# Kernel tuning notes

Hardware: AMD Instinct MI355X
Metric: run time of the kernel (lower is better)

The kernel has to match this reference:

```python
import jax, jax.numpy as jnp
import numpy as np

D_MODEL = 2048
N_HEADS = 16
HEAD_DIM = 128
WINDOW = 512
ROPE_BASE = 10000.0
B, N = 2, 2048
INNER = N_HEADS * HEAD_DIM


def setup_inputs() -> dict:
    key = jax.random.key(0)
    k1, k2, k3 = jax.random.split(key, 3)
    x = jax.random.normal(k1, (B, N, D_MODEL), dtype=jnp.float32)
    # torch nn.Linear stores weight as [out_features, in_features]
    w_qkv = jax.random.normal(k2, (3 * INNER, D_MODEL), dtype=jnp.float32) / np.sqrt(D_MODEL)
    w_o = jax.random.normal(k3, (D_MODEL, INNER), dtype=jnp.float32) / np.sqrt(INNER)
    return {"x": x, "w_qkv": w_qkv, "w_o": w_o}


def _rotate_half(t):
    t1, t2 = jnp.split(t, 2, axis=-1)
    return jnp.concatenate([-t2, t1], axis=-1)


def _rope(q, k, offset=0):
    # q, k: [B, H, N, D]; GPT-NeoX half-split rotary embedding
    D = q.shape[-1]
    inv_freq = 1.0 / (ROPE_BASE ** (jnp.arange(0, D, 2, dtype=jnp.float32) / D))
    pos = jnp.arange(q.shape[2], dtype=jnp.float32) + offset
    ang = pos[:, None] * inv_freq[None, :]                 # [N, D/2]
    cos = jnp.concatenate([jnp.cos(ang), jnp.cos(ang)], axis=-1)  # [N, D]
    sin = jnp.concatenate([jnp.sin(ang), jnp.sin(ang)], axis=-1)
    q_r = q * cos + _rotate_half(q) * sin
    k_r = k * cos + _rotate_half(k) * sin
    return q_r, k_r


def reference(x, w_qkv, w_o):
    Bq, Nq, _ = x.shape
    # QKV projection (no bias)
    qkv = jnp.einsum('bnd,ed->bne', x, w_qkv)              # [B, N, 3*INNER]
    q, k, v = jnp.split(qkv, 3, axis=-1)
    def to_heads(t):
        return t.reshape(Bq, Nq, N_HEADS, HEAD_DIM).transpose(0, 2, 1, 3)  # [B,H,N,D]
    q, k, v = to_heads(q), to_heads(k), to_heads(v)
    q, k = _rope(q, k, offset=0)
    # sliding-window causal mask: valid key j for query i iff (i - WINDOW) < j <= i
    i = jnp.arange(Nq)[:, None]
    j = jnp.arange(Nq)[None, :]
    valid = (j > i - WINDOW) & (j <= i)                    # [N, N]
    scale = 1.0 / np.sqrt(HEAD_DIM)
    scores = jnp.einsum('bhnd,bhkd->bhnk', q, k) * scale   # [B,H,N,N]
    scores = jnp.where(valid[None, None], scores, -jnp.inf)
    att = jax.nn.softmax(scores, axis=-1)
    out = jnp.einsum('bhnk,bhkd->bhnd', att, v)
    out = out.transpose(0, 2, 1, 3).reshape(Bq, Nq, INNER)
    y = jnp.einsum('bni,di->bnd', out, w_o)
    return y
```

## Files before the change

### kernel.cpp

```cpp
#include <hip/hip_runtime.h>
#include <hip/hip_bf16.h>
#include <cstdint>

typedef __bf16 bf16x8 __attribute__((ext_vector_type(8)));
typedef float floatx4 __attribute__((ext_vector_type(4)));

__device__ __forceinline__ void gl2lds16(const void* g, void* l) {
  __builtin_amdgcn_global_load_lds(
      (const __attribute__((address_space(1))) unsigned int*)g,
      (__attribute__((address_space(3))) unsigned int*)(uintptr_t)l,
      16, 0, 0);
}

__global__ __launch_bounds__(256)
void cvt_kernel(const float* __restrict__ in, __hip_bfloat16* __restrict__ out, int n) {
  int i = (blockIdx.x * 256 + threadIdx.x) * 4;
  if (i >= n) return;
  const float4 v = *(const float4*)(in + i);
  out[i + 0] = __float2bfloat16(v.x);
  out[i + 1] = __float2bfloat16(v.y);
  out[i + 2] = __float2bfloat16(v.z);
  out[i + 3] = __float2bfloat16(v.w);
}

__global__ __launch_bounds__(256)
void gemm_bt(const __hip_bfloat16* __restrict__ A, const __hip_bfloat16* __restrict__ Bm,
             void* __restrict__ Cp, int M, int Nc, int K, int c_fp32)
{
  __shared__ __hip_bfloat16 As[128 * 32];
  __shared__ __hip_bfloat16 Bs[128 * 32];
  const int tid = threadIdx.x;
  const int lane = tid & 63, wave = tid >> 6;
  const int wm = (wave & 1) * 64, wn = (wave >> 1) * 64;
  const int m0 = blockIdx.x * 128, n0 = blockIdx.y * 128;
  const int lrow = lane & 15, lk = (lane >> 4) * 8;
  floatx4 acc[4][4] = {};
  const int c0 = tid, c1 = tid + 256;
  const int r0 = c0 >> 2, o0 = (c0 & 3) * 8;
  const int r1 = c1 >> 2, o1 = (c1 & 3) * 8;
  for (int kt = 0; kt < K; kt += 32) {
    __syncthreads();
    gl2lds16(A + (size_t)(m0 + r0) * K + kt + o0, &As[c0 * 8]);
    gl2lds16(A + (size_t)(m0 + r1) * K + kt + o1, &As[c1 * 8]);
    gl2lds16(Bm + (size_t)(n0 + r0) * K + kt + o0, &Bs[c0 * 8]);
    gl2lds16(Bm + (size_t)(n0 + r1) * K + kt + o1, &Bs[c1 * 8]);
    __syncthreads();
    bf16x8 af[4], bfr[4];
#pragma unroll
    for (int t = 0; t < 4; t++) af[t] = *(const bf16x8*)&As[(wm + t * 16 + lrow) * 32 + lk];
#pragma unroll
    for (int t = 0; t < 4; t++) bfr[t] = *(const bf16x8*)&Bs[(wn + t * 16 + lrow) * 32 + lk];
#pragma unroll
    for (int mt = 0; mt < 4; mt++)
#pragma unroll
      for (int nt = 0; nt < 4; nt++)
        acc[mt][nt] = __builtin_amdgcn_mfma_f32_16x16x32_bf16(af[mt], bfr[nt], acc[mt][nt], 0, 0, 0);
  }
  const int lq4 = (lane >> 4) * 4;
#pragma unroll
  for (int mt = 0; mt < 4; mt++)
#pragma unroll
    for (int nt = 0; nt < 4; nt++)
#pragma unroll
      for (int r = 0; r < 4; r++) {
        const int m = m0 + wm + mt * 16 + lq4 + r;
        const int n = n0 + wn + nt * 16 + lrow;
        const float v = acc[mt][nt][r];
        if (c_fp32) ((float*)Cp)[(size_t)m * Nc + n] = v;
        else ((__hip_bfloat16*)Cp)[(size_t)m * Nc + n] = __float2bfloat16(v);
      }
}

__global__ __launch_bounds__(256)
void gemm_qkv_fused(const __hip_bfloat16* __restrict__ A,
                    const __hip_bfloat16* __restrict__ W,
                    __hip_bfloat16* __restrict__ Qr,
                    __hip_bfloat16* __restrict__ Kr,
                    __hip_bfloat16* __restrict__ Vt)
{
  __shared__ alignas(16) char smem[16640];
  __shared__ float invf[64];
  __hip_bfloat16* As = (__hip_bfloat16*)smem;
  __hip_bfloat16* Bs = As + 128 * 32;
  __hip_bfloat16* Cs = (__hip_bfloat16*)smem;
  const int tid = threadIdx.x;
  if (tid < 64) invf[tid] = __expf(-(float)tid * 0.14391156831212787f);
  const int lane = tid & 63, wave = tid >> 6;
  const int wm = (wave & 1) * 64, wn = (wave >> 1) * 64;
  const int m0 = blockIdx.x * 128, n0 = blockIdx.y * 128;
  const int K = 2048;
  const int lrow = lane & 15, lk = (lane >> 4) * 8;
  floatx4 acc[4][4] = {};
  const int c0 = tid, c1 = tid + 256;
  const int r0 = c0 >> 2, o0 = (c0 & 3) * 8;
  const int r1 = c1 >> 2, o1 = (c1 & 3) * 8;
  for (int kt = 0; kt < K; kt += 32) {
    __syncthreads();
    gl2lds16(A + (size_t)(m0 + r0) * K + kt + o0, &As[c0 * 8]);
    gl2lds16(A + (size_t)(m0 + r1) * K + kt + o1, &As[c1 * 8]);
    gl2lds16(W + (size_t)(n0 + r0) * K + kt + o0, &Bs[c0 * 8]);
    gl2lds16(W + (size_t)(n0 + r1) * K + kt + o1, &Bs[c1 * 8]);
    __syncthreads();
    bf16x8 af[4], bfr[4];
#pragma unroll
    for (int t = 0; t < 4; t++) af[t] = *(const bf16x8*)&As[(wm + t * 16 + lrow) * 32 + lk];
#pragma unroll
    for (int t = 0; t < 4; t++) bfr[t] = *(const bf16x8*)&Bs[(wn + t * 16 + lrow) * 32 + lk];
#pragma unroll
    for (int mt = 0; mt < 4; mt++)
#pragma unroll
      for (int nt = 0; nt < 4; nt++)
        acc[mt][nt] = __builtin_amdgcn_mfma_f32_16x16x32_bf16(af[mt], bfr[nt], acc[mt][nt], 0, 0, 0);
  }
  const int lq4 = (lane >> 4) * 4;
  const int seg = n0 >> 11;
  const int h = (n0 & 2047) >> 7;
  const int b = m0 >> 11;
  const int bh = b * 16 + h;
  const int seq0 = m0 & 2047;
  const float qscale = (seg == 0) ? 0.08838834764831845f : 1.0f;
  for (int pass = 0; pass < 2; ++pass) {
    __syncthreads();
    if ((wave & 1) == pass) {
#pragma unroll
      for (int mt = 0; mt < 4; mt++)
#pragma unroll
        for (int nt = 0; nt < 4; nt++)
#pragma unroll
          for (int r = 0; r < 4; r++)
            Cs[(mt * 16 + lq4 + r) * 130 + wn + nt * 16 + lrow] =
                __float2bfloat16(acc[mt][nt][r]);
    }
    __syncthreads();
    if (seg < 2) {
      __hip_bfloat16* Out = seg ? Kr : Qr;
#pragma unroll
      for (int p = 0; p < 2; ++p) {
        const int row = (tid >> 3) + p * 32;
        const int oct = (tid & 7) * 8;
        const int m = m0 + pass * 64 + row;
        const float pos = (float)(m & 2047);
        alignas(16) __hip_bfloat16 lo[8], hi[8];
#pragma unroll
        for (int k2 = 0; k2 < 8; k2++) {
          const float ang = pos * invf[oct + k2];
          float sn, cs2;
          __sincosf(ang, &sn, &cs2);
          const float a  = __bfloat162float(Cs[row * 130 + oct + k2]);
          const float bb = __bfloat162float(Cs[row * 130 + oct + k2 + 64]);
          lo[k2] = __float2bfloat16((a * cs2 - bb * sn) * qscale);
          hi[k2] = __float2bfloat16((bb * cs2 + a * sn) * qscale);
        }
        const size_t ob = ((size_t)bh * 2048 + (size_t)(m & 2047)) * 128;
        *(bf16x8*)&Out[ob + oct]      = *(const bf16x8*)lo;
        *(bf16x8*)&Out[ob + oct + 64] = *(const bf16x8*)hi;
      }
    } else {
#pragma unroll
      for (int p = 0; p < 4; ++p) {
        const int d = (tid >> 3) + p * 32;
        const int s8 = (tid & 7) * 8;
        alignas(16) __hip_bfloat16 tmp[8];
#pragma unroll
        for (int k2 = 0; k2 < 8; k2++) tmp[k2] = Cs[(s8 + k2) * 130 + d];
        const size_t ob = ((size_t)bh * 128 + d) * 2048 + seq0 + pass * 64 + s8;
        *(bf16x8*)&Vt[ob] = *(const bf16x8*)tmp;
      }
    }
  }
}

#define KSTR 136
#define VSTR 72
__global__ __launch_bounds__(512, 4)
void attn_swa(const __hip_bfloat16* __restrict__ Qr, const __hip_bfloat16* __restrict__ Kr,
              const __hip_bfloat16* __restrict__ Vt, __hip_bfloat16* __restrict__ Out)
{
  __shared__ __hip_bfloat16 Ks[64 * KSTR];
  __shared__ __hip_bfloat16 Vs[128 * VSTR];
  __shared__ __hip_bfloat16 Pb[8][16 * VSTR];
  const int qt = blockIdx.x, bh = blockIdx.y;
  const int tid = threadIdx.x, lane = tid & 63, wave = tid >> 6;
  const int lrow = lane & 15, lk = (lane >> 4) * 8, lq4 = (lane >> 4) * 4;
  const int i0 = qt * 128;
  const float NEG_INF = -__builtin_inff();
  const __hip_bfloat16* Qh = Qr + (size_t)bh * 2048 * 128;
  const __hip_bfloat16* Kh = Kr + (size_t)bh * 2048 * 128;
  const __hip_bfloat16* Vh = Vt + (size_t)bh * 128 * 2048;

  const int ck0 = tid, ck1 = tid + 512;
  const int kr0 = ck0 >> 4, kg0 = (ck0 & 15) * 8;
  const int kr1 = ck1 >> 4, kg1 = (ck1 & 15) * 8;
  const int cv0 = tid, cv1 = tid + 512;
  const int vd0 = cv0 >> 3, vc0 = (cv0 & 7) * 8;
  const int vd1 = cv1 >> 3, vc1 = (cv1 & 7) * 8;

  const int iw = i0 + wave * 16 + lrow;
  bf16x8 qf[4];
#pragma unroll
  for (int ks = 0; ks < 4; ks++)
    qf[ks] = *(const bf16x8*)&Qh[(size_t)iw * 128 + ks * 32 + lk];

  floatx4 accO[8] = {};
  float m_i = NEG_INF, l_i = 0.f;
  const int imin = i0 + wave * 16;
  const int lo = i0 - 511;
  const int jt_lo = (lo > 0 ? lo : 0) >> 6;
  const int jt_hi = (i0 + 127) >> 6;

  int j0n = jt_lo * 64;
  int4 rk0 = *(const int4*)&Kh[(size_t)(j0n + kr0) * 128 + kg0];
  int4 rk1 = *(const int4*)&Kh[(size_t)(j0n + kr1) * 128 + kg1];
  int4 rv0 = *(const int4*)&Vh[(size_t)vd0 * 2048 + j0n + vc0];
  int4 rv1 = *(const int4*)&Vh[(size_t)vd1 * 2048 + j0n + vc1];

  for (int jt = jt_lo; jt <= jt_hi; jt++) {
    const int j0 = jt * 64;
    __syncthreads();
    *(int4*)&Ks[kr0 * KSTR + kg0] = rk0;
    *(int4*)&Ks[kr1 * KSTR + kg1] = rk1;
    *(int4*)&Vs[vd0 * VSTR + vc0] = rv0;
    *(int4*)&Vs[vd1 * VSTR + vc1] = rv1;
    if (jt < jt_hi) {
      const int jn = j0 + 64;
      rk0 = *(const int4*)&Kh[(size_t)(jn + kr0) * 128 + kg0];
      rk1 = *(const int4*)&Kh[(size_t)(jn + kr1) * 128 + kg1];
      rv0 = *(const int4*)&Vh[(size_t)vd0 * 2048 + jn + vc0];
      rv1 = *(const int4*)&Vh[(size_t)vd1 * 2048 + jn + vc1];
    }
    asm volatile("" ::: "memory");
    __builtin_amdgcn_s_waitcnt(0xC07F);
    __builtin_amdgcn_s_barrier();
    asm volatile("" ::: "memory");

    floatx4 s[4] = {};
#pragma unroll
    for (int nt = 0; nt < 4; nt++) {
      const int krow = (nt * 16 + lrow) * KSTR;
#pragma unroll
      for (int ks = 0; ks < 4; ks++) {
        const bf16x8 kf = *(const bf16x8*)&Ks[krow + ks * 32 + lk];
        s[nt] = __builtin_amdgcn_mfma_f32_16x16x32_bf16(kf, qf[ks], s[nt], 0, 0, 0);
      }
    }
    const bool full = (j0 + 63 <= imin) && (j0 >= imin + 15 - 511);
    float rmax = NEG_INF;
    if (full) {
#pragma unroll
      for (int nt = 0; nt < 4; nt++)
#pragma unroll
        for (int r = 0; r < 4; r++) rmax = fmaxf(rmax, s[nt][r]);
    } else {
#pragma unroll
      for (int nt = 0; nt < 4; nt++) {
#pragma unroll
        for (int r = 0; r < 4; r++) {
          const int j = j0 + nt * 16 + lq4 + r;
          const float sv = ((j <= iw) && (j > iw - 512)) ? s[nt][r] : NEG_INF;
          s[nt][r] = sv;
          rmax = fmaxf(rmax, sv);
        }
      }
    }
    rmax = fmaxf(rmax, __shfl_xor(rmax, 16));
    rmax = fmaxf(rmax, __shfl_xor(rmax, 32));
    const float mnew = fmaxf(m_i, rmax);
    const float alpha = __expf(fminf(m_i - mnew, 0.f));
    m_i = mnew;
    float rs = 0.f;
    if (full) {
#pragma unroll
      for (int nt = 0; nt < 4; nt++)
#pragma unroll
        for (int r = 0; r < 4; r++) {
          const float p = __expf(s[nt][r] - mnew);
          s[nt][r] = p;
          rs += p;
        }
    } else {
#pragma unroll
      for (int nt = 0; nt < 4; nt++)
#pragma unroll
        for (int r = 0; r < 4; r++) {
          const float sv = s[nt][r];
          const float p = (sv == NEG_INF) ? 0.f : __expf(sv - mnew);
          s[nt][r] = p;
          rs += p;
        }
    }
    rs += __shfl_xor(rs, 16);
    rs += __shfl_xor(rs, 32);
    l_i = l_i * alpha + rs;
#pragma unroll
    for (int dt = 0; dt < 8; dt++) accO[dt] *= alpha;
#pragma unroll
    for (int nt = 0; nt < 4; nt++) {
      alignas(8) __hip_bfloat16 p4[4];
#pragma unroll
      for (int r = 0; r < 4; r++) p4[r] = __float2bfloat16(s[nt][r]);
      *(uint64_t*)&Pb[wave][lrow * VSTR + nt * 16 + lq4] = *(const uint64_t*)p4;
    }
    bf16x8 pf[2];
#pragma unroll
    for (int jf = 0; jf < 2; jf++)
      pf[jf] = *(const bf16x8*)&Pb[wave][lrow * VSTR + jf * 32 + lk];
#pragma unroll
    for (int dt = 0; dt < 8; dt++) {
      const int vrow = (dt * 16 + lrow) * VSTR;
#pragma unroll
      for (int jf = 0; jf < 2; jf++) {
        const bf16x8 vf = *(const bf16x8*)&Vs[vrow + jf * 32 + lk];
        accO[dt] = __builtin_amdgcn_mfma_f32_16x16x32_bf16(vf, pf[jf], accO[dt], 0, 0, 0);
      }
    }
  }
  const int b = bh >> 4, h = bh & 15;
  const float inv_l = 1.0f / l_i;
  const size_t rowb = ((size_t)(b * 2048 + iw)) * 2048 + h * 128;
#pragma unroll
  for (int dt = 0; dt < 8; dt++) {
    alignas(8) __hip_bfloat16 o4[4];
#pragma unroll
    for (int r = 0; r < 4; r++) o4[r] = __float2bfloat16(accO[dt][r] * inv_l);
    *(uint64_t*)&Out[rowb + dt * 16 + lq4] = *(const uint64_t*)o4;
  }
}

extern "C" void kernel_launch(void* const* d_in, const int* in_sizes, int n_in,
                              void* d_out, int out_size, void* d_ws, size_t ws_size,
                              hipStream_t stream)
{
  const float* x = (const float*)d_in[0];
  const float* w_qkv = (const float*)d_in[1];
  const float* w_o = (const float*)d_in[2];
  float* y = (float*)d_out;
  char* ws = (char*)d_ws;

  const size_t SZ_X = 16777216;
  const size_t SZ_WQKV = 25165824;
  const size_t SZ_Q = 16777216;

  __hip_bfloat16* xb = (__hip_bfloat16*)(ws);
  __hip_bfloat16* wqkvb = (__hip_bfloat16*)(ws + SZ_X);
  __hip_bfloat16* Qr = (__hip_bfloat16*)(ws + SZ_X + SZ_WQKV);
  __hip_bfloat16* Kr = (__hip_bfloat16*)(ws + SZ_X + SZ_WQKV + SZ_Q);
  __hip_bfloat16* Vt = (__hip_bfloat16*)(ws + SZ_X + SZ_WQKV + 2 * SZ_Q);

  cvt_kernel<<<dim3(8192), dim3(256), 0, stream>>>(x, xb, 8388608);
  cvt_kernel<<<dim3(12288), dim3(256), 0, stream>>>(w_qkv, wqkvb, 12582912);
  gemm_qkv_fused<<<dim3(32, 48), dim3(256), 0, stream>>>(xb, wqkvb, Qr, Kr, Vt);
  attn_swa<<<dim3(16, 32), dim3(512), 0, stream>>>(Qr, Kr, Vt, xb );
  cvt_kernel<<<dim3(4096), dim3(256), 0, stream>>>(w_o, wqkvb, 4194304);
  gemm_bt<<<dim3(32, 16), dim3(256), 0, stream>>>(xb, wqkvb, (void*)y, 4096, 2048, 2048, 1);
}
```

Baseline: 385.5 us.

## Rewrite QKV GEMM with 256x256 tiles and 4-stage async LDS pipeline

Replaces the 128x128 single-buffered QKV projection GEMM with a 512-thread, 256x256-tile kernel. It uses a 4-deep ring of direct global-to-LDS loads with waitcnt-based barriers, XOR-swizzled LDS layout to avoid bank conflicts, and setprio around the MFMA block. The RoPE/V-transpose epilogue is restructured for the larger tile with vectorized LDS reads. This is meant to hide global load latency and raise arithmetic intensity, at the cost of 128KB dynamic LDS (one block per CU), a grid of only 384 blocks, and hand-tuned vmcnt immediates that must match the number of loads in flight.

```diff
diff --git a/kernel.cpp b/kernel.cpp
--- a/kernel.cpp
+++ b/kernel.cpp
@@ -71,100 +71,138 @@
       }
 }
 
-__global__ __launch_bounds__(256)
-void gemm_qkv_fused(const __hip_bfloat16* __restrict__ A,
-                    const __hip_bfloat16* __restrict__ W,
-                    __hip_bfloat16* __restrict__ Qr,
-                    __hip_bfloat16* __restrict__ Kr,
-                    __hip_bfloat16* __restrict__ Vt)
+__global__ __launch_bounds__(512, 2)
+void gemm_qkv256(const __hip_bfloat16* __restrict__ A,
+                 const __hip_bfloat16* __restrict__ W,
+                 __hip_bfloat16* __restrict__ Qr,
+                 __hip_bfloat16* __restrict__ Kr,
+                 __hip_bfloat16* __restrict__ Vt)
 {
-  __shared__ alignas(16) char smem[16640];
-  __shared__ float invf[64];
-  __hip_bfloat16* As = (__hip_bfloat16*)smem;
-  __hip_bfloat16* Bs = As + 128 * 32;
-  __hip_bfloat16* Cs = (__hip_bfloat16*)smem;
-  const int tid = threadIdx.x;
-  if (tid < 64) invf[tid] = __expf(-(float)tid * 0.14391156831212787f);
-  const int lane = tid & 63, wave = tid >> 6;
-  const int wm = (wave & 1) * 64, wn = (wave >> 1) * 64;
-  const int m0 = blockIdx.x * 128, n0 = blockIdx.y * 128;
-  const int K = 2048;
-  const int lrow = lane & 15, lk = (lane >> 4) * 8;
-  floatx4 acc[4][4] = {};
-  const int c0 = tid, c1 = tid + 256;
-  const int r0 = c0 >> 2, o0 = (c0 & 3) * 8;
-  const int r1 = c1 >> 2, o1 = (c1 & 3) * 8;
-  for (int kt = 0; kt < K; kt += 32) {
-    __syncthreads();
-    gl2lds16(A + (size_t)(m0 + r0) * K + kt + o0, &As[c0 * 8]);
-    gl2lds16(A + (size_t)(m0 + r1) * K + kt + o1, &As[c1 * 8]);
-    gl2lds16(W + (size_t)(n0 + r0) * K + kt + o0, &Bs[c0 * 8]);
-    gl2lds16(W + (size_t)(n0 + r1) * K + kt + o1, &Bs[c1 * 8]);
-    __syncthreads();
-    bf16x8 af[4], bfr[4];
-#pragma unroll
-    for (int t = 0; t < 4; t++) af[t] = *(const bf16x8*)&As[(wm + t * 16 + lrow) * 32 + lk];
-#pragma unroll
-    for (int t = 0; t < 4; t++) bfr[t] = *(const bf16x8*)&Bs[(wn + t * 16 + lrow) * 32 + lk];
-#pragma unroll
-    for (int mt = 0; mt < 4; mt++)
-#pragma unroll
-      for (int nt = 0; nt < 4; nt++)
-        acc[mt][nt] = __builtin_amdgcn_mfma_f32_16x16x32_bf16(af[mt], bfr[nt], acc[mt][nt], 0, 0, 0);
-  }
-  const int lq4 = (lane >> 4) * 4;
+  extern __shared__ __hip_bfloat16 sm[];
+  const int tid = threadIdx.x, lane = tid & 63, wave = tid >> 6;
+  const int wr = wave >> 2, wc = wave & 3;
+  const int m0 = blockIdx.x << 8, n0 = blockIdx.y << 8;
+  const int lrow = lane & 15, dg = lane >> 4, lq4 = dg * 4;
+  const int rslot = (dg ^ ((lrow >> 1) & 3)) * 8;
+
+  const int arow = tid >> 2;
+  const int ascol = ((tid & 3) ^ ((tid >> 3) & 3)) * 8;
+  const __hip_bfloat16* aS0 = A + (size_t)(m0 + arow) * 2048 + ascol;
+  const __hip_bfloat16* aS1 = A + (size_t)(m0 + 128 + arow) * 2048 + ascol;
+  const __hip_bfloat16* bS0 = W + (size_t)(n0 + arow) * 2048 + ascol;
+  const __hip_bfloat16* bS1 = W + (size_t)(n0 + 128 + arow) * 2048 + ascol;
+
+  floatx4 acc[8][4] = {};
+
+#define STAGE(TT) do {                                        \
+    const int bb_ = (TT) & 3; const int kk_ = (TT) * 32;      \
+    gl2lds16(aS0 + kk_, &sm[bb_ * 16384 + tid * 8]);          \
+    gl2lds16(aS1 + kk_, &sm[bb_ * 16384 + 4096 + tid * 8]);   \
+    gl2lds16(bS0 + kk_, &sm[bb_ * 16384 + 8192 + tid * 8]);   \
+    gl2lds16(bS1 + kk_, &sm[bb_ * 16384 + 12288 + tid * 8]);  \
+  } while (0)
+
+  STAGE(0); STAGE(1); STAGE(2);
+
+#define KSTEP(TT, WIMM, DOSTAGE) do {                                          \
+    asm volatile("" ::: "memory");                                             \
+    __builtin_amdgcn_s_waitcnt(WIMM);     \
+    __builtin_amdgcn_s_barrier();       \
+    asm volatile("" ::: "memory");                                             \
+    const int bb = (TT) & 3;                                                   \
+    if (DOSTAGE) STAGE((TT) + 3);                                              \
+    bf16x8 af[8], bfr[4];                                                      \
+    _Pragma("unroll")                                                          \
+    for (int mt = 0; mt < 8; mt++)                                             \
+      af[mt] = *(const bf16x8*)&sm[bb * 16384 + (wr * 128 + mt * 16 + lrow) * 32 + rslot]; \
+    _Pragma("unroll")                                                          \
+    for (int nt = 0; nt < 4; nt++)                                             \
+      bfr[nt] = *(const bf16x8*)&sm[bb * 16384 + 8192 + (wc * 64 + nt * 16 + lrow) * 32 + rslot]; \
+    __builtin_amdgcn_s_setprio(1);                                             \
+    _Pragma("unroll")                                                          \
+    for (int mt = 0; mt < 8; mt++)                                             \
+      _Pragma("unroll")                                                        \
+      for (int nt = 0; nt < 4; nt++)                                           \
+        acc[mt][nt] = __builtin_amdgcn_mfma_f32_16x16x32_bf16(af[mt], bfr[nt], acc[mt][nt], 0, 0, 0); \
+    __builtin_amdgcn_s_setprio(0);                                             \
+  } while (0)
+
+  for (int t = 0; t < 61; ++t) KSTEP(t, 0x78, true);
+  KSTEP(61, 0x78, false);
+  KSTEP(62, 0x74, false);
+  KSTEP(63, 0x70, false);
+#undef KSTEP
+#undef STAGE
+
   const int seg = n0 >> 11;
-  const int h = (n0 & 2047) >> 7;
+  const int h0 = (n0 & 2047) >> 7;
   const int b = m0 >> 11;
-  const int bh = b * 16 + h;
   const int seq0 = m0 & 2047;
-  const float qscale = (seg == 0) ? 0.08838834764831845f : 1.0f;
-  for (int pass = 0; pass < 2; ++pass) {
-    __syncthreads();
-    if ((wave & 1) == pass) {
-#pragma unroll
-      for (int mt = 0; mt < 4; mt++)
-#pragma unroll
-        for (int nt = 0; nt < 4; nt++)
-#pragma unroll
-          for (int r = 0; r < 4; r++)
-            Cs[(mt * 16 + lq4 + r) * 130 + wn + nt * 16 + lrow] =
-                __float2bfloat16(acc[mt][nt][r]);
+  float* invfp = (float*)((char*)sm + 122880);
+
+  __syncthreads();
+  if (seg < 2 && tid < 64) invfp[tid] = __expf(-(float)tid * 0.14391156831212787f);
+
+  const float qs = (seg == 0) ? 0.08838834764831845f : 1.0f;
+  for (int p = 0; p < 2; ++p) {
+    if (p) __syncthreads();
+    if (wr == p) {
+      if (seg < 2) {
+#pragma unroll
+        for (int mt = 0; mt < 8; mt++)
+#pragma unroll
+          for (int nt = 0; nt < 4; nt++)
+#pragma unroll
+            for (int r = 0; r < 4; r++)
+              sm[(mt * 16 + lq4 + r) * 264 + wc * 64 + nt * 16 + lrow] =
+                  __float2bfloat16(acc[mt][nt][r]);
+      } else {
+#pragma unroll
+        for (int mt = 0; mt < 8; mt++)
+#pragma unroll
+          for (int nt = 0; nt < 4; nt++)
+#pragma unroll
+            for (int r = 0; r < 4; r++)
+              sm[(wc * 64 + nt * 16 + lrow) * 136 + mt * 16 + lq4 + r] =
+                  __float2bfloat16(acc[mt][nt][r]);
+      }
     }
     __syncthreads();
     if (seg < 2) {
       __hip_bfloat16* Out = seg ? Kr : Qr;
 #pragma unroll
-      for (int p = 0; p < 2; ++p) {
-        const int row = (tid >> 3) + p * 32;
-        const int oct = (tid & 7) * 8;
-        const int m = m0 + pass * 64 + row;
-        const float pos = (float)(m & 2047);
+      for (int it = 0; it < 4; ++it) {
+        const int task = tid + it * 512;
+        const int row = task >> 4;
+        const int hh = (task >> 3) & 1;
+        const int g8 = (task & 7) * 8;
+        const int seq = seq0 + p * 128 + row;
+        const float pos = (float)seq;
+        const bf16x8 lo8 = *(const bf16x8*)&sm[row * 264 + hh * 128 + g8];
+        const bf16x8 hi8 = *(const bf16x8*)&sm[row * 264 + hh * 128 + g8 + 64];
         alignas(16) __hip_bfloat16 lo[8], hi[8];
 #pragma unroll
-        for (int k2 = 0; k2 < 8; k2++) {
-          const float ang = pos * invf[oct + k2];
-          float sn, cs2;
-          __sincosf(ang, &sn, &cs2);
-          const float a  = __bfloat162float(Cs[row * 130 + oct + k2]);
-          const float bb = __bfloat162float(Cs[row * 130 + oct + k2 + 64]);
-          lo[k2] = __float2bfloat16((a * cs2 - bb * sn) * qscale);
-          hi[k2] = __float2bfloat16((bb * cs2 + a * sn) * qscale);
+        for (int k = 0; k < 8; k++) {
+          float sn, cs;
+          __sincosf(pos * invfp[g8 + k], &sn, &cs);
+          const float a = (float)lo8[k];
+          const float bb2 = (float)hi8[k];
+          lo[k] = __float2bfloat16((a * cs - bb2 * sn) * qs);
+          hi[k] = __float2bfloat16((bb2 * cs + a * sn) * qs);
         }
-        const size_t ob = ((size_t)bh * 2048 + (size_t)(m & 2047)) * 128;
-        *(bf16x8*)&Out[ob + oct]      = *(const bf16x8*)lo;
-        *(bf16x8*)&Out[ob + oct + 64] = *(const bf16x8*)hi;
+        const size_t ob = ((size_t)((b * 16 + h0 + hh) * 2048 + seq)) * 128;
+        *(bf16x8*)&Out[ob + g8] = *(const bf16x8*)lo;
+        *(bf16x8*)&Out[ob + g8 + 64] = *(const bf16x8*)hi;
       }
     } else {
 #pragma unroll
-      for (int p = 0; p < 4; ++p) {
-        const int d = (tid >> 3) + p * 32;
-        const int s8 = (tid & 7) * 8;
-        alignas(16) __hip_bfloat16 tmp[8];
-#pragma unroll
-        for (int k2 = 0; k2 < 8; k2++) tmp[k2] = Cs[(s8 + k2) * 130 + d];
-        const size_t ob = ((size_t)bh * 128 + d) * 2048 + seq0 + pass * 64 + s8;
-        *(bf16x8*)&Vt[ob] = *(const bf16x8*)tmp;
+      for (int it = 0; it < 8; ++it) {
+        const int task = tid + it * 512;
+        const int col = task >> 4;
+        const int sg = (task & 15) * 8;
+        const bf16x8 v8 = *(const bf16x8*)&sm[col * 136 + sg];
+        const int hh = col >> 7, d = col & 127;
+        *(bf16x8*)&Vt[((size_t)((b * 16 + h0 + hh) * 128 + d)) * 2048 + seq0 + p * 128 + sg] = v8;
       }
     }
   }
@@ -346,9 +384,16 @@
   __hip_bfloat16* Kr = (__hip_bfloat16*)(ws + SZ_X + SZ_WQKV + SZ_Q);
   __hip_bfloat16* Vt = (__hip_bfloat16*)(ws + SZ_X + SZ_WQKV + 2 * SZ_Q);
 
+  static bool s_attr_done = false;
+  if (!s_attr_done) {
+    hipFuncSetAttribute((const void*)gemm_qkv256,
+                        hipFuncAttributeMaxDynamicSharedMemorySize, 131072);
+    s_attr_done = true;
+  }
+
   cvt_kernel<<<dim3(8192), dim3(256), 0, stream>>>(x, xb, 8388608);
   cvt_kernel<<<dim3(12288), dim3(256), 0, stream>>>(w_qkv, wqkvb, 12582912);
-  gemm_qkv_fused<<<dim3(32, 48), dim3(256), 0, stream>>>(xb, wqkvb, Qr, Kr, Vt);
+  gemm_qkv256<<<dim3(16, 24), dim3(512), 131072, stream>>>(xb, wqkvb, Qr, Kr, Vt);
   attn_swa<<<dim3(16, 32), dim3(512), 0, stream>>>(Qr, Kr, Vt, xb );
   cvt_kernel<<<dim3(4096), dim3(256), 0, stream>>>(w_o, wqkvb, 4194304);
   gemm_bt<<<dim3(32, 16), dim3(256), 0, stream>>>(xb, wqkvb, (void*)y, 4096, 2048, 2048, 1);
```

After: 363.5 us. 5.7% less time.
